# Performance work log

Hardware: AMD Instinct MI355X
Metric: run time of the kernel (lower is better)

Reference implementation:

```python
import jax, jax.numpy as jnp
import numpy as np

D = 2048        # d_model == d_enc
S = 8192        # encoder sequence length
V = 32000 + 2   # vocab_size + 2
R = 7           # num_rel


def _gru_cell(x, h, Wih, Whh, bih, bhh):
    # torch.nn.GRUCell gate order: r, z, n
    gi = x @ Wih.T + bih          # [3D]
    gh = h @ Whh.T + bhh          # [3D]
    ir, iz, inn = jnp.split(gi, 3)
    hr, hz, hn = jnp.split(gh, 3)
    r = jax.nn.sigmoid(ir + hr)
    z = jax.nn.sigmoid(iz + hz)
    n = jnp.tanh(inn + r * hn)
    return (1.0 - z) * n + z * h


def setup_inputs() -> dict:
    key = jax.random.key(0)
    ks = jax.random.split(key, 28)
    s = 1.0 / np.sqrt(D)
    def u(k, shape, scale=s):
        return jax.random.uniform(k, shape, jnp.float32, -scale, scale)
    inp = {
        "enc_tokens":    jax.random.normal(ks[0], (S, D), jnp.float32),
        "c_prev":        jax.random.normal(ks[1], (D,), jnp.float32),
        "partner_embed": jax.random.normal(ks[2], (D,), jnp.float32),
        "cov_vec":       jax.random.normal(ks[3], (D,), jnp.float32),
        # gru_alpha
        "Wih_a": u(ks[4], (3 * D, D)), "Whh_a": u(ks[5], (3 * D, D)),
        "bih_a": u(ks[6], (3 * D,)),   "bhh_a": u(ks[7], (3 * D,)),
        # gru_beta
        "Wih_b": u(ks[8], (3 * D, D)), "Whh_b": u(ks[9], (3 * D, D)),
        "bih_b": u(ks[10], (3 * D,)),  "bhh_b": u(ks[11], (3 * D,)),
        # attention projections
        "W_enc": u(ks[12], (D, D)), "b_enc": u(ks[13], (D,)),
        "W_co":  u(ks[14], (D, D)), "b_co":  u(ks[15], (D,)),
        "W_cov": u(ks[16], (D, D)), "b_cov": u(ks[17], (D,)),
        "W_score": u(ks[18], (1, D)), "b_score": u(ks[19], (1,)),
        # heads
        "W_sym": u(ks[20], (V, D)), "b_sym": u(ks[21], (V,)),
        "W_rel": u(ks[22], (R, D)), "b_rel": u(ks[23], (R,)),
    }
    return inp


def reference(enc_tokens, c_prev, partner_embed, cov_vec,
              Wih_a, Whh_a, bih_a, bhh_a,
              Wih_b, Whh_b, bih_b, bhh_b,
              W_enc, b_enc, W_co, b_co, W_cov, b_cov,
              W_score, b_score, W_sym, b_sym, W_rel, b_rel):
    # alpha GRU step
    c_o = _gru_cell(partner_embed, c_prev, Wih_a, Whh_a, bih_a, bhh_a)  # [D]
    # additive (Bahdanau) attention
    e = enc_tokens @ W_enc.T + b_enc              # [S, D]
    co = c_o @ W_co.T + b_co                      # [D] broadcast over S
    cov = cov_vec @ W_cov.T + b_cov               # [D]
    scores = jnp.tanh(e + co + cov) @ W_score[0] + b_score[0]  # [S]
    alpha = jax.nn.softmax(scores)                # [S]
    ctx = alpha @ enc_tokens                      # [D]
    # beta GRU step
    c_beta = _gru_cell(ctx, c_o, Wih_b, Whh_b, bih_b, bhh_b)  # [D]
    symbol_logits = c_beta @ W_sym.T + b_sym      # [V]
    rel_logits = c_beta @ W_rel.T + b_rel         # [R]
    return (symbol_logits, rel_logits, c_beta, alpha)
```

## Files before the change

kernel.cpp:

```cpp
#include <hip/hip_runtime.h>
#include <hip/hip_bf16.h>
#include <math.h>

#define DD 2048
#define SS 8192
#define VV 32002
#define RR 7
#define GATE 6144

typedef unsigned short u16;
typedef __attribute__((ext_vector_type(8))) unsigned short u16x8;
typedef __attribute__((ext_vector_type(8))) short bfrag;
typedef __attribute__((ext_vector_type(4))) float f32x4;

__device__ __attribute__((aligned(256))) u16 g_ah[(size_t)SS * DD];
__device__ __attribute__((aligned(256))) u16 g_bh[(size_t)DD * DD];
__device__ __attribute__((aligned(256))) float g_gia[GATE], g_gha[GATE], g_gib[GATE], g_ghb[GATE];
__device__ __attribute__((aligned(256))) float g_co[DD], g_cc[DD], g_ctx[DD], g_cb[DD];
__device__ __attribute__((aligned(256))) float g_alpha[SS];
__device__ __attribute__((aligned(256))) float g_scores[SS];

__device__ __forceinline__ float fsigmoid(float x) { return 1.0f / (1.0f + __expf(-x)); }
__device__ __forceinline__ float ftanh(float x)    { return 1.0f - 2.0f / (__expf(2.0f * x) + 1.0f); }
__device__ __forceinline__ u16 f2bf(float v) {
    union { float f; unsigned int i; } c; c.f = v;
    return (u16)((c.i + 0x7FFF + ((c.i >> 16) & 1)) >> 16);
}
__device__ __forceinline__ float bf2f(u16 u) {
    union { unsigned int i; float f; } c; c.i = ((unsigned int)u) << 16; return c.f;
}
__device__ __forceinline__ void gload16(const void* g, void* l) {
    __builtin_amdgcn_global_load_lds(
        (const __attribute__((address_space(1))) void*)g,
        (__attribute__((address_space(3))) void*)l, 16, 0, 0);
}

__global__ void diag_k(float* out, float v) { out[0] = v; }

__global__ __launch_bounds__(256) void presplit_all_k(const float* __restrict__ enc,
                                                      const float* __restrict__ wenc) {
    int b = blockIdx.x;
    const float* src;
    u16* dst;
    size_t i;
    if (b < SS) { src = enc;  dst = g_ah; i = ((size_t)b * 256 + threadIdx.x) * 8; }
    else        { src = wenc; dst = g_bh; i = ((size_t)(b - SS) * 256 + threadIdx.x) * 8; }
    f32x4 v0 = *(const f32x4*)&src[i];
    f32x4 v1 = *(const f32x4*)&src[i + 4];
    u16x8 h;
#pragma unroll
    for (int e = 0; e < 4; ++e) { h[e] = f2bf(v0[e]); h[4 + e] = f2bf(v1[e]); }
    *(u16x8*)&dst[i] = h;
    if (b >= SS) {
        int gt = (b - SS) * 256 + threadIdx.x;
        if (gt < SS) g_scores[gt] = 0.0f;
        if (gt < DD) g_ctx[gt] = 0.0f;
    }
}

template<int PAIR>
__global__ __launch_bounds__(256) void matvec2_k(const float* __restrict__ W0,
                                                 const float* __restrict__ W1,
                                                 const float* __restrict__ x0_in,
                                                 const float* __restrict__ x1_in,
                                                 const float* __restrict__ b0,
                                                 const float* __restrict__ b1) {
    const int half = blockIdx.x >= (GATE / 4);
    const float* W    = half ? W1 : W0;
    const float* bias = half ? b1 : b0;
    const float* x;
    float* out;
    if (PAIR == 0) { x = half ? x1_in : x0_in; out = half ? g_gha : g_gia; }
    else           { x = half ? g_co  : g_ctx; out = half ? g_ghb : g_gib; }
    int wv = threadIdx.x >> 6, lane = threadIdx.x & 63;
    int row = (blockIdx.x - half * (GATE / 4)) * 4 + wv;
    const float* wp = W + (size_t)row * DD;
    float acc = 0.0f;
#pragma unroll
    for (int j = 0; j < 4; ++j) {
        int base = j * 512 + lane * 8;
        f32x4 w0 = *(const f32x4*)&wp[base];
        f32x4 w1 = *(const f32x4*)&wp[base + 4];
        f32x4 x0 = *(const f32x4*)&x[base];
        f32x4 x1 = *(const f32x4*)&x[base + 4];
#pragma unroll
        for (int e = 0; e < 4; ++e) acc += w0[e] * x0[e] + w1[e] * x1[e];
    }
#pragma unroll
    for (int o = 1; o < 64; o <<= 1) acc += __shfl_xor(acc, o);
    if (lane == 0) out[row] = acc + bias[row];
}

template<int B>
__global__ void gru_out_k(const float* __restrict__ h_in, float* __restrict__ out_f) {
    const float* gi = B ? g_gib : g_gia;
    const float* gh = B ? g_ghb : g_gha;
    int d = blockIdx.x * 256 + threadIdx.x;
    float hh = B ? g_co[d] : h_in[d];
    float r = fsigmoid(gi[d] + gh[d]);
    float z = fsigmoid(gi[DD + d] + gh[DD + d]);
    float n = ftanh(gi[2 * DD + d] + r * gh[2 * DD + d]);
    float c = (1.0f - z) * n + z * hh;
    if (B) { g_cb[d] = c; out_f[d] = c; }
    else   { g_co[d] = c; }
}

__global__ __launch_bounds__(256) void cc_k(const float* __restrict__ Wco, const float* __restrict__ Wcov,
                                            const float* __restrict__ cov,
                                            const float* __restrict__ benc, const float* __restrict__ bco,
                                            const float* __restrict__ bcov) {
    int wv = threadIdx.x >> 6, lane = threadIdx.x & 63;
    int row = blockIdx.x * 4 + wv;
    const float* p1 = Wco + (size_t)row * DD;
    const float* p2 = Wcov + (size_t)row * DD;
    float acc = 0.0f;
#pragma unroll
    for (int j = 0; j < 4; ++j) {
        int base = j * 512 + lane * 8;
        f32x4 u0 = *(const f32x4*)&p1[base];
        f32x4 u1 = *(const f32x4*)&p1[base + 4];
        f32x4 v0 = *(const f32x4*)&p2[base];
        f32x4 v1 = *(const f32x4*)&p2[base + 4];
        f32x4 a0 = *(const f32x4*)&g_co[base];
        f32x4 a1 = *(const f32x4*)&g_co[base + 4];
        f32x4 b0 = *(const f32x4*)&cov[base];
        f32x4 b1 = *(const f32x4*)&cov[base + 4];
#pragma unroll
        for (int e = 0; e < 4; ++e)
            acc += u0[e] * a0[e] + u1[e] * a1[e] + v0[e] * b0[e] + v1[e] * b1[e];
    }
#pragma unroll
    for (int o = 1; o < 64; o <<= 1) acc += __shfl_xor(acc, o);
    if (lane == 0) g_cc[row] = acc + benc[row] + bco[row] + bcov[row];
}

__global__ __launch_bounds__(256) void score_gemm_k(const float* __restrict__ Wsc) {
    __shared__ u16 As[2][128 * 32];
    __shared__ u16 Bs[2][128 * 32];
    const int bid = blockIdx.x;
    const int swz = (bid & 7) * 128 + (bid >> 3);
    const int bm = swz >> 4;
    const int bn = swz & 15;
    const int tid = threadIdx.x;
    const int wave = tid >> 6, lane = tid & 63;
    const int wr = wave >> 1, wc = wave & 1;
    const int srow = lane >> 2;
    const int scol = (((lane & 3) ^ ((lane >> 4) & 3)) * 8);
    const int rsel = lane & 15;
    const int kq = (((lane >> 4) ^ ((lane >> 2) & 3)) * 8);
    const int c0 = wave * 2, c1 = wave * 2 + 1;

    f32x4 acc[4][4];
#pragma unroll
    for (int m = 0; m < 4; ++m)
#pragma unroll
        for (int n = 0; n < 4; ++n) acc[m][n] = f32x4{0.f, 0.f, 0.f, 0.f};

    const u16* gA = g_ah + (size_t)(bm * 128) * DD;
    const u16* gB = g_bh + (size_t)(bn * 128) * DD;
    const size_t off0 = (size_t)(c0 * 16 + srow) * DD + scol;
    const size_t off1 = (size_t)(c1 * 16 + srow) * DD + scol;

    gload16(gA + off0, &As[0][c0 * 512]);
    gload16(gA + off1, &As[0][c1 * 512]);
    gload16(gB + off0, &Bs[0][c0 * 512]);
    gload16(gB + off1, &Bs[0][c1 * 512]);

    int cur = 0;
    for (int step = 0; step < 64; ++step) {
        if (step < 63) {
            size_t k1 = (size_t)(step + 1) * 32;
            gload16(gA + off0 + k1, &As[cur ^ 1][c0 * 512]);
            gload16(gA + off1 + k1, &As[cur ^ 1][c1 * 512]);
            gload16(gB + off0 + k1, &Bs[cur ^ 1][c0 * 512]);
            gload16(gB + off1 + k1, &Bs[cur ^ 1][c1 * 512]);
            asm volatile("s_waitcnt vmcnt(4)" ::: "memory");
        } else {
            asm volatile("s_waitcnt vmcnt(0)" ::: "memory");
        }
        __builtin_amdgcn_s_barrier();
        __builtin_amdgcn_sched_barrier(0);
        bfrag a[4], b[4];
#pragma unroll
        for (int m = 0; m < 4; ++m) a[m] = *(const bfrag*)&As[cur][(wr * 64 + m * 16 + rsel) * 32 + kq];
#pragma unroll
        for (int n = 0; n < 4; ++n) b[n] = *(const bfrag*)&Bs[cur][(wc * 64 + n * 16 + rsel) * 32 + kq];
#pragma unroll
        for (int m = 0; m < 4; ++m)
#pragma unroll
            for (int n = 0; n < 4; ++n)
                acc[m][n] = __builtin_amdgcn_mfma_f32_16x16x32_bf16(a[m], b[n], acc[m][n], 0, 0, 0);
        __builtin_amdgcn_s_barrier();
        __builtin_amdgcn_sched_barrier(0);
        cur ^= 1;
    }

    const int cl = lane & 15, gq = lane >> 4;
    float ccv[4], wv[4];
#pragma unroll
    for (int nf = 0; nf < 4; ++nf) {
        int n = bn * 128 + wc * 64 + nf * 16 + cl;
        ccv[nf] = g_cc[n];
        wv[nf] = Wsc[n];
    }
#pragma unroll
    for (int m = 0; m < 4; ++m) {
#pragma unroll
        for (int r = 0; r < 4; ++r) {
            float v = 0.0f;
#pragma unroll
            for (int nf = 0; nf < 4; ++nf) v += ftanh(acc[m][nf][r] + ccv[nf]) * wv[nf];
            v += __shfl_xor(v, 1); v += __shfl_xor(v, 2);
            v += __shfl_xor(v, 4); v += __shfl_xor(v, 8);
            if (cl == 0) atomicAdd(&g_scores[bm * 128 + wr * 64 + m * 16 + gq * 4 + r], v);
        }
    }
}

__global__ __launch_bounds__(1024) void softmax_k(float* __restrict__ out_alpha) {
    __shared__ float red[16];
    __shared__ float sval;
    int t = threadIdx.x, lane = t & 63, w = t >> 6;
    float loc[8];
    float m = -1e30f;
#pragma unroll
    for (int i = 0; i < 8; ++i) {
        loc[i] = g_scores[t + i * 1024];
        m = fmaxf(m, loc[i]);
    }
#pragma unroll
    for (int o = 1; o < 64; o <<= 1) m = fmaxf(m, __shfl_xor(m, o));
    if (lane == 0) red[w] = m;
    __syncthreads();
    if (t == 0) { float mm = red[0]; for (int i = 1; i < 16; ++i) mm = fmaxf(mm, red[i]); sval = mm; }
    __syncthreads();
    float mx = sval, s = 0.0f;
#pragma unroll
    for (int i = 0; i < 8; ++i) { loc[i] = __expf(loc[i] - mx); s += loc[i]; }
#pragma unroll
    for (int o = 1; o < 64; o <<= 1) s += __shfl_xor(s, o);
    if (lane == 0) red[w] = s;
    __syncthreads();
    if (t == 0) { float ss = 0; for (int i = 0; i < 16; ++i) ss += red[i]; sval = ss; }
    __syncthreads();
    float inv = 1.0f / sval;
#pragma unroll
    for (int i = 0; i < 8; ++i) {
        float a = loc[i] * inv;
        g_alpha[t + i * 1024] = a;
        out_alpha[t + i * 1024] = a;
    }
}

__global__ __launch_bounds__(256) void ctx_partial_k() {
    int t = threadIdx.x, b = blockIdx.x;
    int d0 = t * 8;
    float acc[8] = {0, 0, 0, 0, 0, 0, 0, 0};
    int s0 = b * 64;
    for (int s = s0; s < s0 + 64; ++s) {
        u16x8 v = *(const u16x8*)&g_ah[(size_t)s * DD + d0];
        float a = g_alpha[s];
#pragma unroll
        for (int e = 0; e < 8; ++e) acc[e] += a * bf2f(v[e]);
    }
#pragma unroll
    for (int e = 0; e < 8; ++e) atomicAdd(&g_ctx[d0 + e], acc[e]);
}

__global__ __launch_bounds__(256) void heads_k(const float* __restrict__ Wsym, const float* __restrict__ bsym,
                                               const float* __restrict__ Wrel, const float* __restrict__ brel,
                                               float* __restrict__ out) {
    int wv = threadIdx.x >> 6, lane = threadIdx.x & 63;
    int row = blockIdx.x * 4 + wv;
    if (row >= VV + RR) return;
    const float* wp;
    float bb;
    if (row < VV) { wp = Wsym + (size_t)row * DD; bb = bsym[row]; }
    else          { wp = Wrel + (size_t)(row - VV) * DD; bb = brel[row - VV]; }
    float acc = 0.0f;
#pragma unroll
    for (int j = 0; j < 4; ++j) {
        int base = j * 512 + lane * 8;
        f32x4 w0 = *(const f32x4*)&wp[base];
        f32x4 w1 = *(const f32x4*)&wp[base + 4];
        f32x4 x0 = *(const f32x4*)&g_cb[base];
        f32x4 x1 = *(const f32x4*)&g_cb[base + 4];
#pragma unroll
        for (int e = 0; e < 4; ++e) acc += w0[e] * x0[e] + w1[e] * x1[e];
    }
#pragma unroll
    for (int o = 1; o < 64; o <<= 1) acc += __shfl_xor(acc, o);
    if (lane == 0) out[row] = acc + bb;
}

extern "C" void kernel_launch(void* const* d_in, const int* in_sizes, int n_in,
                              void* d_out, int out_size, void* d_ws, size_t ws_size,
                              hipStream_t stream) {
    float* out = (float*)d_out;

    static const int expected[24] = {
        SS * DD, DD, DD, DD,
        3 * DD * DD, 3 * DD * DD, 3 * DD, 3 * DD,
        3 * DD * DD, 3 * DD * DD, 3 * DD, 3 * DD,
        DD * DD, DD, DD * DD, DD, DD * DD, DD,
        DD, 1, VV * DD, VV, RR * DD, RR
    };
    if (n_in != 24) { diag_k<<<1, 1, 0, stream>>>(out, 4.0e7f); return; }
    for (int i = 0; i < 24; ++i)
        if (in_sizes[i] != expected[i]) { diag_k<<<1, 1, 0, stream>>>(out, 3.0e7f + (i + 1) * 1.0e5f); return; }

    const float* enc     = (const float*)d_in[0];
    const float* cprev   = (const float*)d_in[1];
    const float* partner = (const float*)d_in[2];
    const float* cov     = (const float*)d_in[3];
    const float* Wih_a   = (const float*)d_in[4];
    const float* Whh_a   = (const float*)d_in[5];
    const float* bih_a   = (const float*)d_in[6];
    const float* bhh_a   = (const float*)d_in[7];
    const float* Wih_b   = (const float*)d_in[8];
    const float* Whh_b   = (const float*)d_in[9];
    const float* bih_b   = (const float*)d_in[10];
    const float* bhh_b   = (const float*)d_in[11];
    const float* W_enc   = (const float*)d_in[12];
    const float* b_enc   = (const float*)d_in[13];
    const float* W_co    = (const float*)d_in[14];
    const float* b_co    = (const float*)d_in[15];
    const float* W_cov   = (const float*)d_in[16];
    const float* b_cov   = (const float*)d_in[17];
    const float* W_score = (const float*)d_in[18];
    const float* W_sym   = (const float*)d_in[20];
    const float* b_sym   = (const float*)d_in[21];
    const float* W_rel   = (const float*)d_in[22];
    const float* b_rel   = (const float*)d_in[23];

    presplit_all_k<<<SS + DD * DD / (256 * 8), 256, 0, stream>>>(enc, W_enc);
    matvec2_k<0><<<2 * (GATE / 4), 256, 0, stream>>>(Wih_a, Whh_a, partner, cprev, bih_a, bhh_a);
    gru_out_k<0><<<8, 256, 0, stream>>>(cprev, nullptr);
    cc_k<<<DD / 4, 256, 0, stream>>>(W_co, W_cov, cov, b_enc, b_co, b_cov);
    score_gemm_k<<<1024, 256, 0, stream>>>(W_score);
    softmax_k<<<1, 1024, 0, stream>>>(out + VV + RR + DD);
    ctx_partial_k<<<128, 256, 0, stream>>>();
    matvec2_k<1><<<2 * (GATE / 4), 256, 0, stream>>>(Wih_b, Whh_b, nullptr, nullptr, bih_b, bhh_b);
    gru_out_k<1><<<8, 256, 0, stream>>>(cprev, out + VV + RR);
    heads_k<<<(VV + RR + 3) / 4, 256, 0, stream>>>(W_sym, b_sym, W_rel, b_rel, out);
}
```

Baseline: 263.7 us.

## Enlarge score GEMM tiles to 256x256 with 8 waves and new LDS swizzle

The score GEMM moves from 128x128 tiles with 4 waves to 256x256 tiles with 8 waves per block, each wave computing a 128x64 sub-tile. Global-to-LDS loads are reorganised into per-thread 16-byte chunks with an XOR swizzle keyed on row, and the block-index swizzle is dropped. The aim is to halve global/L2 traffic per FLOP and raise MFMA density. The cost is more accumulator registers and LDS, and only 256 blocks on a 256-CU device, which lowers occupancy and latency hiding.

```diff
diff --git a/kernel.cpp b/kernel.cpp
--- a/kernel.cpp
+++ b/kernel.cpp
@@ -134,59 +134,66 @@
     if (lane == 0) g_cc[row] = acc + benc[row] + bco[row] + bcov[row];
 }
 
-__global__ __launch_bounds__(256) void score_gemm_k(const float* __restrict__ Wsc) {
-    __shared__ u16 As[2][128 * 32];
-    __shared__ u16 Bs[2][128 * 32];
+__global__ __launch_bounds__(512) void score_gemm_k(const float* __restrict__ Wsc) {
+    __shared__ u16 As[2][256 * 32];
+    __shared__ u16 Bs[2][256 * 32];
     const int bid = blockIdx.x;
-    const int swz = (bid & 7) * 128 + (bid >> 3);
-    const int bm = swz >> 4;
-    const int bn = swz & 15;
+    const int bn = bid & 7;
+    const int bm = bid >> 3;
     const int tid = threadIdx.x;
     const int wave = tid >> 6, lane = tid & 63;
-    const int wr = wave >> 1, wc = wave & 1;
-    const int srow = lane >> 2;
-    const int scol = (((lane & 3) ^ ((lane >> 4) & 3)) * 8);
+    const int wr = wave >> 2, wc = wave & 3;
     const int rsel = lane & 15;
-    const int kq = (((lane >> 4) ^ ((lane >> 2) & 3)) * 8);
-    const int c0 = wave * 2, c1 = wave * 2 + 1;
-
-    f32x4 acc[4][4];
-#pragma unroll
-    for (int m = 0; m < 4; ++m)
+    const int lch = lane >> 4;
+
+    f32x4 acc[8][4];
+#pragma unroll
+    for (int m = 0; m < 8; ++m)
 #pragma unroll
         for (int n = 0; n < 4; ++n) acc[m][n] = f32x4{0.f, 0.f, 0.f, 0.f};
 
-    const u16* gA = g_ah + (size_t)(bm * 128) * DD;
-    const u16* gB = g_bh + (size_t)(bn * 128) * DD;
-    const size_t off0 = (size_t)(c0 * 16 + srow) * DD + scol;
-    const size_t off1 = (size_t)(c1 * 16 + srow) * DD + scol;
-
-    gload16(gA + off0, &As[0][c0 * 512]);
-    gload16(gA + off1, &As[0][c1 * 512]);
-    gload16(gB + off0, &Bs[0][c0 * 512]);
-    gload16(gB + off1, &Bs[0][c1 * 512]);
+    const u16* gA = g_ah + (size_t)(bm * 256) * DD;
+    const u16* gB = g_bh + (size_t)(bn * 256) * DD;
+
+    const int c0 = tid, c1 = tid + 512;
+    const int r0 = c0 >> 2, ch0 = c0 & 3;
+    const int r1 = c1 >> 2, ch1 = c1 & 3;
+    const size_t ga0 = (size_t)r0 * DD + ((ch0 ^ ((r0 >> 1) & 3)) * 8);
+    const size_t ga1 = (size_t)r1 * DD + ((ch1 ^ ((r1 >> 1) & 3)) * 8);
+
+    gload16(gA + ga0, &As[0][c0 * 8]);
+    gload16(gA + ga1, &As[0][c1 * 8]);
+    gload16(gB + ga0, &Bs[0][c0 * 8]);
+    gload16(gB + ga1, &Bs[0][c1 * 8]);
 
     int cur = 0;
     for (int step = 0; step < 64; ++step) {
         if (step < 63) {
             size_t k1 = (size_t)(step + 1) * 32;
-            gload16(gA + off0 + k1, &As[cur ^ 1][c0 * 512]);
-            gload16(gA + off1 + k1, &As[cur ^ 1][c1 * 512]);
-            gload16(gB + off0 + k1, &Bs[cur ^ 1][c0 * 512]);
-            gload16(gB + off1 + k1, &Bs[cur ^ 1][c1 * 512]);
+            gload16(gA + ga0 + k1, &As[cur ^ 1][c0 * 8]);
+            gload16(gA + ga1 + k1, &As[cur ^ 1][c1 * 8]);
+            gload16(gB + ga0 + k1, &Bs[cur ^ 1][c0 * 8]);
+            gload16(gB + ga1 + k1, &Bs[cur ^ 1][c1 * 8]);
             asm volatile("s_waitcnt vmcnt(4)" ::: "memory");
         } else {
             asm volatile("s_waitcnt vmcnt(0)" ::: "memory");
         }
         __builtin_amdgcn_s_barrier();
         __builtin_amdgcn_sched_barrier(0);
-        bfrag a[4], b[4];
-#pragma unroll
-        for (int m = 0; m < 4; ++m) a[m] = *(const bfrag*)&As[cur][(wr * 64 + m * 16 + rsel) * 32 + kq];
-#pragma unroll
-        for (int n = 0; n < 4; ++n) b[n] = *(const bfrag*)&Bs[cur][(wc * 64 + n * 16 + rsel) * 32 + kq];
-#pragma unroll
-        for (int m = 0; m < 4; ++m)
+        const int pch = (lch ^ ((rsel >> 1) & 3)) * 8;
+        bfrag a[8], b[4];
+#pragma unroll
+        for (int m = 0; m < 8; ++m) {
+            int row = wr * 128 + m * 16 + rsel;
+            a[m] = *(const bfrag*)&As[cur][row * 32 + pch];
+        }
+#pragma unroll
+        for (int n = 0; n < 4; ++n) {
+            int row = wc * 64 + n * 16 + rsel;
+            b[n] = *(const bfrag*)&Bs[cur][row * 32 + pch];
+        }
+#pragma unroll
+        for (int m = 0; m < 8; ++m)
 #pragma unroll
             for (int n = 0; n < 4; ++n)
                 acc[m][n] = __builtin_amdgcn_mfma_f32_16x16x32_bf16(a[m], b[n], acc[m][n], 0, 0, 0);
@@ -199,12 +206,12 @@
     float ccv[4], wv[4];
 #pragma unroll
     for (int nf = 0; nf < 4; ++nf) {
-        int n = bn * 128 + wc * 64 + nf * 16 + cl;
+        int n = bn * 256 + wc * 64 + nf * 16 + cl;
         ccv[nf] = g_cc[n];
         wv[nf] = Wsc[n];
     }
 #pragma unroll
-    for (int m = 0; m < 4; ++m) {
+    for (int m = 0; m < 8; ++m) {
 #pragma unroll
         for (int r = 0; r < 4; ++r) {
             float v = 0.0f;
@@ -212,7 +219,7 @@
             for (int nf = 0; nf < 4; ++nf) v += ftanh(acc[m][nf][r] + ccv[nf]) * wv[nf];
             v += __shfl_xor(v, 1); v += __shfl_xor(v, 2);
             v += __shfl_xor(v, 4); v += __shfl_xor(v, 8);
-            if (cl == 0) atomicAdd(&g_scores[bm * 128 + wr * 64 + m * 16 + gq * 4 + r], v);
+            if (cl == 0) atomicAdd(&g_scores[bm * 256 + wr * 128 + m * 16 + gq * 4 + r], v);
         }
     }
 }
@@ -337,7 +344,7 @@
     matvec2_k<0><<<2 * (GATE / 4), 256, 0, stream>>>(Wih_a, Whh_a, partner, cprev, bih_a, bhh_a);
     gru_out_k<0><<<8, 256, 0, stream>>>(cprev, nullptr);
     cc_k<<<DD / 4, 256, 0, stream>>>(W_co, W_cov, cov, b_enc, b_co, b_cov);
-    score_gemm_k<<<1024, 256, 0, stream>>>(W_score);
+    score_gemm_k<<<256, 512, 0, stream>>>(W_score);
     softmax_k<<<1, 1024, 0, stream>>>(out + VV + RR + DD);
     ctx_partial_k<<<128, 256, 0, stream>>>();
     matvec2_k<1><<<2 * (GATE / 4), 256, 0, stream>>>(Wih_b, Whh_b, nullptr, nullptr, bih_b, bhh_b);
```

Measured after the change: 238.3 us. -9.6%, faster.
